# Performance work log

Measured on AMD Instinct MI355X. Metric: run time of the kernel, lower is better.

The kernel has to match this reference:

```python
import jax, jax.numpy as jnp
import numpy as np

B, L, W = 128, 8192, 31

def setup_inputs() -> dict:
    key = jax.random.key(0)
    x = jax.random.normal(key, (B, L), dtype=jnp.float32)
    return {"x": x, "win_size": W}

def reference(x, win_size):
    # Sliding-window unfold: out[b, i, j] = x[b, i + j] for i in [0, L-2r), j in [0, win_size)
    r = win_size // 2
    L_ = x.shape[1]
    n_win = L_ - 2 * r  # number of window-center positions
    idx = jnp.arange(n_win)[:, None] + jnp.arange(win_size)[None, :]  # [n_win, W]
    return x[:, idx]  # [B, n_win, W]
```

## Files before the change

kernel.cpp:

```cpp
#include <hip/hip_runtime.h>


constexpr int B_   = 128;
constexpr int L_   = 8192;
constexpr int W_   = 31;
constexpr int NWIN = L_ - (W_ - 1);
constexpr int PERB = NWIN * W_;
constexpr long long TOTAL = (long long)B_ * PERB;
constexpr int NVEC  = (int)(TOTAL / 4);
constexpr int BLOCK = 256;
constexpr int K     = 4;
constexpr int CHUNK = BLOCK * K;
constexpr int GRID  = (NVEC + CHUNK - 1) / CHUNK;

typedef float f32x4 __attribute__((ext_vector_type(4)));

__global__ __launch_bounds__(BLOCK) void unfold_kernel(const float* __restrict__ x,
                                                       float* __restrict__ out) {
    unsigned t = blockIdx.x * CHUNK + threadIdx.x;
    unsigned o = t << 2;
    unsigned b = o / (unsigned)PERB;
    unsigned q = o - b * (unsigned)PERB;
    unsigned i = q / 31u;
    unsigned j = q - 31u * i;
    const float* __restrict__ xb = x + b * L_;
    f32x4* __restrict__ o4 = reinterpret_cast<f32x4*>(out);

#pragma unroll
    for (int s = 0; s < K; ++s) {
        if (t < (unsigned)NVEC) {
            f32x4 v;
            unsigned base = i + j;
#pragma unroll
            for (int k = 0; k < 4; ++k) {
                unsigned jk  = j + (unsigned)k;
                unsigned idx = base + (unsigned)k - (jk >= 31u ? 30u : 0u);
                float val;
                if (q + (unsigned)k >= (unsigned)PERB) {
                    val = xb[L_ + (q + (unsigned)k - (unsigned)PERB)];
                } else {
                    val = xb[idx];
                }
                v[k] = val;
            }
            o4[t] = v;
        }
        t += BLOCK;
        q += 1024u;
        i += 33u;
        j += 1u;
        if (j >= 31u) { j -= 31u; ++i; }
        if (q >= (unsigned)PERB) {
            q -= (unsigned)PERB;
            xb += L_;
            i = q / 31u;
            j = q - 31u * i;
        }
    }
}

extern "C" void kernel_launch(void* const* d_in, const int* in_sizes, int n_in,
                              void* d_out, int out_size, void* d_ws, size_t ws_size,
                              hipStream_t stream) {
    const float* x = (const float*)d_in[0];
    float* out = (float*)d_out;
    unfold_kernel<<<GRID, BLOCK, 0, stream>>>(x, out);
}
```

Baseline: 146.4 us.

## Stage each block's input span in LDS before emitting unfolded windows

Each block first loads into shared memory the contiguous slice of the input row that its output chunk covers, plus the start of the next row when the chunk straddles a batch boundary. It then builds the output vectors from LDS instead of issuing repeated scattered global loads per element. This removes redundant global/L2 read traffic for overlapping windows, but adds a block-wide barrier and more index bookkeeping. The kernel is dominated by output writes, so the benefit may be limited.

```diff
diff --git a/kernel.cpp b/kernel.cpp
--- a/kernel.cpp
+++ b/kernel.cpp
@@ -12,49 +12,75 @@
 constexpr int K     = 4;
 constexpr int CHUNK = BLOCK * K;
 constexpr int GRID  = (NVEC + CHUNK - 1) / CHUNK;
+constexpr int ELEMS = CHUNK * 4;
+constexpr int SPAN  = 168;
 
 typedef float f32x4 __attribute__((ext_vector_type(4)));
 
 __global__ __launch_bounds__(BLOCK) void unfold_kernel(const float* __restrict__ x,
                                                        float* __restrict__ out) {
+    __shared__ float lds[2 * SPAN];
+
+    const unsigned o0 = blockIdx.x * (unsigned)ELEMS;
+    const unsigned b  = o0 / (unsigned)PERB;
+    const unsigned q0 = o0 - b * (unsigned)PERB;
+    const unsigned qL = (q0 + (unsigned)ELEMS - 1u < (unsigned)PERB - 1u)
+                        ? (q0 + (unsigned)ELEMS - 1u) : ((unsigned)PERB - 1u);
+    const unsigned i_lo = q0 / 31u;
+    const unsigned i_hi = qL / 31u;
+    const unsigned n0   = i_hi - i_lo + 31u;
+
+    const float* __restrict__ xb = x + b * L_;
+    for (unsigned k = threadIdx.x; k < n0; k += BLOCK)
+        lds[k] = xb[i_lo + k];
+
+    const bool straddle = (q0 + (unsigned)ELEMS > (unsigned)PERB) &&
+                          (b + 1u < (unsigned)B_);
+    if (straddle) {
+        unsigned q1max = q0 + (unsigned)ELEMS - 1u - (unsigned)PERB;
+        unsigned n1 = q1max / 31u + 31u;
+        const float* __restrict__ xb1 = xb + L_;
+        for (unsigned k = threadIdx.x; k < n1; k += BLOCK)
+            lds[SPAN + k] = xb1[k];
+    }
+    __syncthreads();
+
     unsigned t = blockIdx.x * CHUNK + threadIdx.x;
-    unsigned o = t << 2;
-    unsigned b = o / (unsigned)PERB;
-    unsigned q = o - b * (unsigned)PERB;
+    unsigned q = q0 + 4u * threadIdx.x;
+    unsigned boff = 0, ibase = i_lo;
+    bool sel1 = false;
+    if (q >= (unsigned)PERB) {
+        q -= (unsigned)PERB; sel1 = true; boff = SPAN; ibase = 0;
+    }
     unsigned i = q / 31u;
     unsigned j = q - 31u * i;
-    const float* __restrict__ xb = x + b * L_;
     f32x4* __restrict__ o4 = reinterpret_cast<f32x4*>(out);
 
 #pragma unroll
     for (int s = 0; s < K; ++s) {
         if (t < (unsigned)NVEC) {
             f32x4 v;
-            unsigned base = i + j;
+            unsigned idx0 = boff + (i + j - ibase);
 #pragma unroll
             for (int k = 0; k < 4; ++k) {
                 unsigned jk  = j + (unsigned)k;
-                unsigned idx = base + (unsigned)k - (jk >= 31u ? 30u : 0u);
-                float val;
-                if (q + (unsigned)k >= (unsigned)PERB) {
-                    val = xb[L_ + (q + (unsigned)k - (unsigned)PERB)];
-                } else {
-                    val = xb[idx];
-                }
-                v[k] = val;
+                unsigned idx = idx0 + (unsigned)k - (jk >= 31u ? 30u : 0u);
+                if (!sel1 && q + (unsigned)k >= (unsigned)PERB)
+                    idx = (unsigned)SPAN + (q + (unsigned)k - (unsigned)PERB);
+                v[k] = lds[idx];
             }
             o4[t] = v;
         }
         t += BLOCK;
         q += 1024u;
-        i += 33u;
-        j += 1u;
-        if (j >= 31u) { j -= 31u; ++i; }
-        if (q >= (unsigned)PERB) {
+        if (!sel1 && q >= (unsigned)PERB) {
             q -= (unsigned)PERB;
-            xb += L_;
+            sel1 = true; boff = SPAN; ibase = 0;
             i = q / 31u;
             j = q - 31u * i;
+        } else {
+            i += 33u; j += 1u;
+            if (j >= 31u) { j -= 31u; ++i; }
         }
     }
 }
```

Result: faster. 132.0 us, median of 2 (-9.9%).
